# Optimization experiments

Measured on AMD Instinct MI355X. Metric: run time of the kernel, lower is better.

## Reference

```python
import jax, jax.numpy as jnp
import numpy as np

KEEP_H = 0.9   # zoneout_h keep prob (eval: deterministic mix)
KEEP_C = 0.5   # zoneout_c keep prob
F_BIAS = 1.0   # forget gate bias
EPS = 1e-5


def _ln(x, g, b):
    mu = x.mean(-1, keepdims=True)
    v = x.var(-1, keepdims=True)
    return (x - mu) * jax.lax.rsqrt(v + EPS) * g + b


def _ln4(z, g, b, h):
    # layer-norm each of the 4 gate chunks independently
    B = z.shape[0]
    z4 = z.reshape(B, 4, h)
    mu = z4.mean(-1, keepdims=True)
    v = z4.var(-1, keepdims=True)
    zn = ((z4 - mu) * jax.lax.rsqrt(v + EPS)).reshape(B, 4 * h)
    return zn * g + b


def _ln_lstm_cell(x, h, c, W, b, gg, bg, gc, bc):
    hu = h.shape[1]
    z = _ln4(jnp.concatenate([x, h], axis=1) @ W + b, gg, bg, hu)
    i, j, f, o = jnp.split(z, 4, axis=1)
    new_c = c * jax.nn.sigmoid(f + F_BIAS) + jax.nn.sigmoid(i) * jnp.tanh(j)
    new_h = jnp.tanh(_ln(new_c, gc, bc)) * jax.nn.sigmoid(o)
    # zoneout, eval mode (deterministic expectation)
    new_h = KEEP_H * new_h + (1.0 - KEEP_H) * h
    new_c = KEEP_C * new_c + (1.0 - KEEP_C) * c
    return new_h, new_c


def setup_inputs() -> dict:
    key = jax.random.key(0)
    ks = jax.random.split(key, 6)
    B, T, E, F, S, V = 128, 100, 128, 700, 400, 10000
    w = lambda k, shape: (jax.random.normal(k, shape, jnp.float32) * 0.06)
    return {
        "inputs": jax.random.normal(ks[0], (B, T, E), jnp.float32),
        "W0": w(ks[1], (E + F, 4 * F)), "b0": jnp.zeros((4 * F,), jnp.float32),
        "g0": jnp.ones((4 * F,), jnp.float32), "bg0": jnp.zeros((4 * F,), jnp.float32),
        "gc0": jnp.ones((F,), jnp.float32), "bc0": jnp.zeros((F,), jnp.float32),
        "W1": w(ks[2], (S + F, 4 * F)), "b1": jnp.zeros((4 * F,), jnp.float32),
        "g1": jnp.ones((4 * F,), jnp.float32), "bg1": jnp.zeros((4 * F,), jnp.float32),
        "gc1": jnp.ones((F,), jnp.float32), "bc1": jnp.zeros((F,), jnp.float32),
        "WS": w(ks[3], (F + S, 4 * S)), "bS": jnp.zeros((4 * S,), jnp.float32),
        "gS": jnp.ones((4 * S,), jnp.float32), "bgS": jnp.zeros((4 * S,), jnp.float32),
        "gcS": jnp.ones((S,), jnp.float32), "bcS": jnp.zeros((S,), jnp.float32),
        "Wout": w(ks[4], (F, V)), "bout": jnp.zeros((V,), jnp.float32),
    }


def reference(inputs, W0, b0, g0, bg0, gc0, bc0,
              W1, b1, g1, bg1, gc1, bc1,
              WS, bS, gS, bgS, gcS, bcS, Wout, bout):
    B, T, E = inputs.shape
    F = gc0.shape[0]
    S = gcS.shape[0]
    xs = inputs.transpose(1, 0, 2)  # [T, B, E]
    init = (jnp.zeros((B, F), inputs.dtype), jnp.zeros((B, F), inputs.dtype),
            jnp.zeros((B, S), inputs.dtype), jnp.zeros((B, S), inputs.dtype))

    def step(carry, xt):
        fh, fc, sh, sc = carry
        fh, fc = _ln_lstm_cell(xt, fh, fc, W0, b0, g0, bg0, gc0, bc0)  # Fast cell 0
        sh, sc = _ln_lstm_cell(fh, sh, sc, WS, bS, gS, bgS, gcS, bcS)  # Slow cell
        fh, fc = _ln_lstm_cell(sh, fh, fc, W1, b1, g1, bg1, gc1, bc1)  # Fast cell 1
        return (fh, fc, sh, sc), fh

    (fh, fc, sh, sc), outs = jax.lax.scan(step, init, xs)  # outs: [T, B, F]
    # torch: cat(outputs, dim=1).view(-1, F) == reshape of [B, T, F]
    flat = outs.transpose(1, 0, 2).reshape(B * T, F)
    logits = (flat @ Wout + bout).reshape(T, B, -1)  # torch .view([T, B, V])
    return (logits, fh, fc, sh, sc)
```

## Files before the change

### kernel.cpp

```cpp
#include <hip/hip_runtime.h>
#include <math.h>


#define B_ 128
#define T_ 100
#define E_ 128
#define F_ 700
#define S_ 400
#define V_ 10000

#define FP_ 704
#define SP_ 416
#define G_  256
#define TPB_ 512

#define W0_TILE_B 45056
#define KW_TILE_B 71680
#define LDS_BYTES 143360

using v8s = __attribute__((ext_vector_type(8))) short;
using v4f = __attribute__((ext_vector_type(4))) float;
typedef unsigned short u16;

#define NTL(p)    __builtin_nontemporal_load((p))

__device__ __forceinline__ void stcohf(float* p, float v) {
    asm volatile("global_store_dword %0, %1, off sc0 sc1" :: "v"(p), "v"(v) : "memory");
}
__device__ __forceinline__ void stcohs(u16* p, u16 v) {
    unsigned w = v;
    asm volatile("global_store_short %0, %1, off sc0 sc1" :: "v"(p), "v"(w) : "memory");
}

__device__ __forceinline__ u16 f2bf(float x) {
    unsigned int u = __float_as_uint(x);
    u += 0x7FFFu + ((u >> 16) & 1u);
    return (u16)(u >> 16);
}
__device__ __forceinline__ float bf2f(u16 h) {
    return __uint_as_float(((unsigned int)h) << 16);
}
__device__ __forceinline__ void split3f(float x, u16& h, u16& m, u16& l) {
    h = f2bf(x); float r  = x - bf2f(h);
    m = f2bf(r); float r2 = r - bf2f(m);
    l = f2bf(r2);
}
__device__ __forceinline__ float sigm(float x) { return 1.0f / (1.0f + expf(-x)); }

__device__ __forceinline__ void gbar(unsigned* flags, unsigned* go, unsigned target) {
    asm volatile("s_waitcnt vmcnt(0)" ::: "memory");
    __syncthreads();
    if (threadIdx.x == 0) {
        __hip_atomic_store(flags + (size_t)blockIdx.x * 16, target,
                           __ATOMIC_RELAXED, __HIP_MEMORY_SCOPE_AGENT);
        asm volatile("buffer_inv sc0 sc1" ::: "memory");
    }
    if (blockIdx.x == 0) {
        if (threadIdx.x < G_) {
            const unsigned* f = flags + (size_t)threadIdx.x * 16;
            while (__hip_atomic_load(f, __ATOMIC_RELAXED, __HIP_MEMORY_SCOPE_AGENT) < target)
                __builtin_amdgcn_s_sleep(1);
        }
        __syncthreads();
        if (threadIdx.x == 0)
            __hip_atomic_store(go, target, __ATOMIC_RELAXED, __HIP_MEMORY_SCOPE_AGENT);
    } else {
        if (threadIdx.x == 0) {
            while (__hip_atomic_load(go, __ATOMIC_RELAXED, __HIP_MEMORY_SCOPE_AGENT) < target)
                __builtin_amdgcn_s_sleep(1);
        }
    }
    __syncthreads();
}

__global__ __launch_bounds__(256) void wtrans3(
    const float* __restrict__ W, int K, int N,
    u16* __restrict__ WtH, u16* __restrict__ WtM, u16* __restrict__ WtL,
    int Kp, int K1, int K1pad)
{
    __shared__ float t[32][33];
    const int c0 = blockIdx.x * 32, kp0 = blockIdx.y * 32;
    const int tx = threadIdx.x & 31, ty = threadIdx.x >> 5;
    #pragma unroll
    for (int i = 0; i < 4; ++i) {
        int kpos = kp0 + ty + i * 8, c = c0 + tx;
        int k = (kpos < K1) ? kpos : (kpos >= K1pad ? K1 + (kpos - K1pad) : -1);
        t[ty + i * 8][tx] = (k >= 0 && k < K && c < N) ? W[(size_t)k * N + c] : 0.f;
    }
    __syncthreads();
    #pragma unroll
    for (int i = 0; i < 4; ++i) {
        int r = c0 + ty + i * 8;
        u16 h, m, l;
        split3f(t[tx][ty + i * 8], h, m, l);
        size_t idx = (size_t)r * Kp + kp0 + tx;
        WtH[idx] = h; WtM[idx] = m; WtL[idx] = l;
    }
}

__global__ __launch_bounds__(256) void wtrans(
    const float* __restrict__ W, int K, int N,
    u16* __restrict__ Wt, int Kpad)
{
    __shared__ float t[32][33];
    const int c0 = blockIdx.x * 32, k0 = blockIdx.y * 32;
    const int tx = threadIdx.x & 31, ty = threadIdx.x >> 5;
    #pragma unroll
    for (int i = 0; i < 4; ++i) {
        int k = k0 + ty + i * 8, c = c0 + tx;
        t[ty + i * 8][tx] = (k < K && c < N) ? W[(size_t)k * N + c] : 0.f;
    }
    __syncthreads();
    #pragma unroll
    for (int i = 0; i < 4; ++i) {
        int r = c0 + ty + i * 8;
        Wt[(size_t)r * Kpad + k0 + tx] = f2bf(t[tx][ty + i * 8]);
    }
}

__global__ __launch_bounds__(512, 1) void zxpre(
    const float* __restrict__ inputs,
    const u16* __restrict__ WH, const u16* __restrict__ WM,
    const u16* __restrict__ WL, const float* __restrict__ b0,
    float* __restrict__ zx)
{
    const int lane = threadIdx.x & 63, wid = threadIdx.x >> 6;
    const int lo = lane & 15, hi = lane >> 4;
    const int ntiles = 175 * 100;
    for (int i = blockIdx.x * 8 + wid; i < ntiles; i += gridDim.x * 8) {
        const int t = i / 175, ct = i % 175;
        v4f acc[8];
        #pragma unroll
        for (int m = 0; m < 8; ++m) acc[m] = (v4f)0.f;
        const size_t bb = (size_t)(ct * 16 + lo) * 832 + hi * 8;
        for (int kt = 0; kt < 4; ++kt) {
            const size_t bo = bb + kt * 32;
            v8s bh = *(const v8s*)(WH + bo);
            v8s bm = *(const v8s*)(WM + bo);
            v8s bl = *(const v8s*)(WL + bo);
            #pragma unroll
            for (int m = 0; m < 8; ++m) {
                const float* p = inputs + (size_t)(m * 16 + lo) * (T_ * E_)
                               + (size_t)t * E_ + kt * 32 + hi * 8;
                float v0[8];
                *(float4*)(v0)     = *(const float4*)(p);
                *(float4*)(v0 + 4) = *(const float4*)(p + 4);
                v8s ah, am, al;
                #pragma unroll
                for (int j = 0; j < 8; ++j) {
                    u16 H, M, L; split3f(v0[j], H, M, L);
                    ah[j] = (short)H; am[j] = (short)M; al[j] = (short)L;
                }
                acc[m] = __builtin_amdgcn_mfma_f32_16x16x32_bf16(ah, bh, acc[m], 0, 0, 0);
                acc[m] = __builtin_amdgcn_mfma_f32_16x16x32_bf16(ah, bm, acc[m], 0, 0, 0);
                acc[m] = __builtin_amdgcn_mfma_f32_16x16x32_bf16(am, bh, acc[m], 0, 0, 0);
                acc[m] = __builtin_amdgcn_mfma_f32_16x16x32_bf16(ah, bl, acc[m], 0, 0, 0);
                acc[m] = __builtin_amdgcn_mfma_f32_16x16x32_bf16(al, bh, acc[m], 0, 0, 0);
                acc[m] = __builtin_amdgcn_mfma_f32_16x16x32_bf16(am, bm, acc[m], 0, 0, 0);
            }
        }
        const int col = ct * 16 + lo;
        const float bb0 = b0[col];
        #pragma unroll
        for (int m = 0; m < 8; ++m)
            #pragma unroll
            for (int r = 0; r < 4; ++r) {
                int row = m * 16 + hi * 4 + r;
                zx[((size_t)t * B_ + row) * 2800 + col] = acc[m][r] + bb0;
            }
    }
}

__device__ void fill_tile(char* dst, const u16* __restrict__ H,
                          const u16* __restrict__ M, int Kp, int gcol0, int NT)
{
    const int n = 16 * NT * 4;
    for (int idx = threadIdx.x; idx < n; idx += TPB_) {
        const int c   = idx & 3;
        const int kt  = (idx >> 2) % NT;
        const int col = (idx >> 2) / NT;
        const size_t g = (size_t)(gcol0 + col) * Kp + kt * 32 + c * 8;
        const int o = kt * 2048 + col * 64 + c * 16;
        *(v8s*)(dst + o)        = *(const v8s*)(H + g);
        *(v8s*)(dst + o + 1024) = *(const v8s*)(M + g);
    }
}

__device__ void gemm_lds(
    const char* lt, int NT,
    const u16* __restrict__ A1H, const u16* __restrict__ A1M,
    const u16* __restrict__ A1L, int lda1, int K1pad,
    const u16* __restrict__ A2H, const u16* __restrict__ A2M,
    const u16* __restrict__ A2L, int lda2,
    const u16* __restrict__ WL, int KpL, int col0,
    const float* __restrict__ bias, const float* __restrict__ zadd,
    float* __restrict__ z, int N)
{
    const int lane = threadIdx.x & 63;
    const int lo = lane & 15, hi = lane >> 4;
    const int r0 = (threadIdx.x >> 6) * 16;
    v4f acc = (v4f)0.f;
    const u16* blp = WL + (size_t)(col0 + lo) * KpL + hi * 8;
    const size_t arow = (size_t)(r0 + lo);

    v8s aH[3], aM[3], aL[3], bL[3];
    #pragma unroll
    for (int s = 0; s < 3; ++s) {
        const int kb2 = s * 32;
        const bool s1 = kb2 < K1pad;
        const size_t ao = arow * (s1 ? lda1 : lda2)
                        + (s1 ? kb2 : kb2 - K1pad) + hi * 8;
        aH[s] = *(const v8s*)((s1 ? A1H : A2H) + ao);
        aM[s] = *(const v8s*)((s1 ? A1M : A2M) + ao);
        aL[s] = *(const v8s*)((s1 ? A1L : A2L) + ao);
        bL[s] = *(const v8s*)(blp + kb2);
    }

    for (int kt0 = 0; kt0 < NT; kt0 += 3) {
        #pragma unroll
        for (int j = 0; j < 3; ++j) {
            const int kt = kt0 + j;
            if (kt < NT) {
                const int lb = kt * 2048 + lo * 64 + hi * 16;
                v8s bh = *(const v8s*)(lt + lb);
                v8s bm = *(const v8s*)(lt + lb + 1024);
                acc = __builtin_amdgcn_mfma_f32_16x16x32_bf16(aH[j], bh,    acc, 0, 0, 0);
                acc = __builtin_amdgcn_mfma_f32_16x16x32_bf16(aH[j], bm,    acc, 0, 0, 0);
                acc = __builtin_amdgcn_mfma_f32_16x16x32_bf16(aM[j], bh,    acc, 0, 0, 0);
                acc = __builtin_amdgcn_mfma_f32_16x16x32_bf16(aH[j], bL[j], acc, 0, 0, 0);
                acc = __builtin_amdgcn_mfma_f32_16x16x32_bf16(aL[j], bh,    acc, 0, 0, 0);
                acc = __builtin_amdgcn_mfma_f32_16x16x32_bf16(aM[j], bm,    acc, 0, 0, 0);
                const int kn = kt + 3;
                if (kn < NT) {
                    const int kb2 = kn * 32;
                    const bool s1 = kb2 < K1pad;
                    const size_t ao = arow * (s1 ? lda1 : lda2)
                                    + (s1 ? kb2 : kb2 - K1pad) + hi * 8;
                    aH[j] = *(const v8s*)((s1 ? A1H : A2H) + ao);
                    aM[j] = *(const v8s*)((s1 ? A1M : A2M) + ao);
                    aL[j] = *(const v8s*)((s1 ? A1L : A2L) + ao);
                    bL[j] = *(const v8s*)(blp + kb2);
                }
            }
        }
    }

    const int col = col0 + lo;
    if (zadd) {
        #pragma unroll
        for (int r = 0; r < 4; ++r) {
            int row = r0 + hi * 4 + r;
            float za = NTL(&zadd[(size_t)row * N + col]);
            stcohf(&z[(size_t)row * N + col], acc[r] + za);
        }
    } else {
        const float bv = bias[col];
        #pragma unroll
        for (int r = 0; r < 4; ++r) {
            int row = r0 + hi * 4 + r;
            stcohf(&z[(size_t)row * N + col], acc[r] + bv);
        }
    }
}

template <int NV>
__device__ __forceinline__ void blockSumN(float* v, float* red) {
    const int w = threadIdx.x >> 6, lane = threadIdx.x & 63;
    #pragma unroll
    for (int k = 0; k < NV; ++k) {
        float x = v[k];
        #pragma unroll
        for (int off = 32; off > 0; off >>= 1) x += __shfl_down(x, off, 64);
        v[k] = x;
    }
    __syncthreads();
    if (lane == 0) {
        #pragma unroll
        for (int k = 0; k < NV; ++k) red[k * 8 + w] = v[k];
    }
    __syncthreads();
    #pragma unroll
    for (int k = 0; k < NV; ++k) {
        float r = 0.f;
        #pragma unroll
        for (int j = 0; j < 8; ++j) r += red[k * 8 + j];
        v[k] = r;
    }
    __syncthreads();
}

template <int FF>
__device__ void pw_phase(const float* __restrict__ z,
    const float* __restrict__ gg, const float* __restrict__ bg,
    const float* __restrict__ gc, const float* __restrict__ bc,
    float* __restrict__ h, float* __restrict__ c,
    u16* __restrict__ hpH, u16* __restrict__ hpM, u16* __restrict__ hpL,
    int hstride, u16* __restrict__ hist, int t, float* red)
{
    const int tid = threadIdx.x;
    constexpr int NU = (FF + TPB_ - 1) / TPB_;
    for (int b = blockIdx.x; b < B_; b += G_) {
        const float* zr = z + (size_t)b * 4 * FF;
        float* hr = h + (size_t)b * FF;
        float* cr = c + (size_t)b * FF;

        float sv[8] = {0, 0, 0, 0, 0, 0, 0, 0};
        #pragma unroll
        for (int i = 0; i < NU; ++i) {
            int u = tid + i * TPB_;
            if (u < FF) {
                #pragma unroll
                for (int g = 0; g < 4; ++g) {
                    float v = NTL(&zr[g * FF + u]);
                    sv[g] += v; sv[4 + g] += v * v;
                }
            }
        }
        blockSumN<8>(sv, red);
        float mu[4], rs[4];
        #pragma unroll
        for (int g = 0; g < 4; ++g) {
            mu[g] = sv[g] / FF;
            rs[g] = rsqrtf(sv[4 + g] / FF - mu[g] * mu[g] + 1e-5f);
        }

        float nc[NU], og[NU], ho[NU], co[NU];
        float cv[2] = {0, 0};
        #pragma unroll
        for (int i = 0; i < NU; ++i) {
            int u = tid + i * TPB_;
            if (u < FF) {
                float zi = (NTL(&zr[u])          - mu[0]) * rs[0] * gg[u]          + bg[u];
                float zj = (NTL(&zr[FF + u])     - mu[1]) * rs[1] * gg[FF + u]     + bg[FF + u];
                float zf = (NTL(&zr[2 * FF + u]) - mu[2]) * rs[2] * gg[2 * FF + u] + bg[2 * FF + u];
                float zo = (NTL(&zr[3 * FF + u]) - mu[3]) * rs[3] * gg[3 * FF + u] + bg[3 * FF + u];
                float cold = cr[u];
                float ncv = cold * sigm(zf + 1.0f) + sigm(zi) * tanhf(zj);
                nc[i] = ncv; og[i] = sigm(zo); co[i] = cold; ho[i] = hr[u];
                cv[0] += ncv; cv[1] += ncv * ncv;
            } else { nc[i] = 0.f; og[i] = 0.f; co[i] = 0.f; ho[i] = 0.f; }
        }
        blockSumN<2>(cv, red);
        float muc = cv[0] / FF;
        float rsc = rsqrtf(cv[1] / FF - muc * muc + 1e-5f);

        #pragma unroll
        for (int i = 0; i < NU; ++i) {
            int u = tid + i * TPB_;
            if (u < FF) {
                float nh = tanhf((nc[i] - muc) * rsc * gc[u] + bc[u]) * og[i];
                float hout = 0.9f * nh + 0.1f * ho[i];
                float cout = 0.5f * nc[i] + 0.5f * co[i];
                stcohf(&hr[u], hout);
                stcohf(&cr[u], cout);
                u16 H, M, L;
                split3f(hout, H, M, L);
                size_t po = (size_t)b * hstride + u;
                stcohs(&hpH[po], H); stcohs(&hpM[po], M); stcohs(&hpL[po], L);
                if (hist) stcohs(&hist[((size_t)b * T_ + t) * FP_ + u], H);
            }
        }
        if (hist && tid < FP_ - FF)
            stcohs(&hist[((size_t)b * T_ + t) * FP_ + FF + tid], (u16)0);
    }
}

__global__ __launch_bounds__(TPB_) void mega(
    const float* __restrict__ b0, const float* __restrict__ g0,
    const float* __restrict__ bg0, const float* __restrict__ gc0,
    const float* __restrict__ bc0,
    const float* __restrict__ b1, const float* __restrict__ g1,
    const float* __restrict__ bg1, const float* __restrict__ gc1,
    const float* __restrict__ bc1,
    const float* __restrict__ bS, const float* __restrict__ gS,
    const float* __restrict__ bgS, const float* __restrict__ gcS,
    const float* __restrict__ bcS,
    const float* __restrict__ zx,
    float* fh, float* fc, float* sh, float* sc, float* z, u16* hist,
    u16* fhH, u16* fhM, u16* fhL, u16* shH, u16* shM, u16* shL,
    u16* W0H, u16* W0M, u16* W0L, u16* WSH, u16* WSM, u16* WSL,
    u16* W1H, u16* W1M, u16* W1L,
    float* outTail, unsigned* flags, unsigned* go)
{
    extern __shared__ char lds[];
    __shared__ float red[64];
    const int b = blockIdx.x;
    const int gtid = blockIdx.x * TPB_ + threadIdx.x;
    unsigned tgt = 0;

    if (b <= 174) {
        fill_tile(lds, W0H + 128, W0M + 128, 832, b * 16, 22);
        if (b <= 155) fill_tile(lds + W0_TILE_B, W1H, W1M, 1120, b * 16, 35);
        else          fill_tile(lds + W0_TILE_B, WSH, WSM, 1120, (b - 156) * 16, 35);
    } else {
        fill_tile(lds, WSH, WSM, 1120, (b - 156) * 16, 35);
        if (b <= 193)
            fill_tile(lds + KW_TILE_B, W1H, W1M, 1120, (156 + b - 175) * 16, 35);
    }
    __syncthreads();

    for (int t = 0; t < T_; ++t) {
        if (b <= 174)
            gemm_lds(lds, 22,
                     fhH, fhM, fhL, FP_, FP_, fhH, fhM, fhL, FP_,
                     W0L + 128, 832, b * 16,
                     nullptr, zx + (size_t)t * B_ * 2800, z, 2800);
        gbar(flags, go, ++tgt);
        pw_phase<F_>(z, g0, bg0, gc0, bc0, fh, fc, fhH, fhM, fhL, FP_, nullptr, 0, red);
        gbar(flags, go, ++tgt);
        if (b >= 156)
            gemm_lds(lds + (b <= 174 ? W0_TILE_B : 0), 35,
                     fhH, fhM, fhL, FP_, FP_, shH, shM, shL, SP_,
                     WSL, 1120, (b - 156) * 16,
                     bS, nullptr, z, 1600);
        gbar(flags, go, ++tgt);
        pw_phase<S_>(z, gS, bgS, gcS, bcS, sh, sc, shH, shM, shL, SP_, nullptr, 0, red);
        gbar(flags, go, ++tgt);
        if (b <= 155)
            gemm_lds(lds + W0_TILE_B, 35,
                     shH, shM, shL, SP_, SP_, fhH, fhM, fhL, FP_,
                     W1L, 1120, b * 16, b1, nullptr, z, 2800);
        else if (b >= 175 && b <= 193)
            gemm_lds(lds + KW_TILE_B, 35,
                     shH, shM, shL, SP_, SP_, fhH, fhM, fhL, FP_,
                     W1L, 1120, (156 + b - 175) * 16, b1, nullptr, z, 2800);
        gbar(flags, go, ++tgt);
        pw_phase<F_>(z, g1, bg1, gc1, bc1, fh, fc, fhH, fhM, fhL, FP_, hist, t, red);
        gbar(flags, go, ++tgt);
    }

    const int NF = B_ * F_, NS = B_ * S_;
    for (int i = gtid; i < 2 * NF + 2 * NS; i += G_ * TPB_) {
        float v = (i < NF) ? fh[i] : (i < 2 * NF) ? fc[i - NF]
                : (i < 2 * NF + NS) ? sh[i - 2 * NF] : sc[i - 2 * NF - NS];
        stcohf(&outTail[i], v);
    }
}

__global__ __launch_bounds__(512) void ogemm(
    const u16* __restrict__ A, const u16* __restrict__ Bt,
    const float* __restrict__ bias, float* __restrict__ C)
{
    const int N = V_;
    const int tid = threadIdx.x, lane = tid & 63, wid = tid >> 6;
    const int wm = wid >> 1, wn = wid & 1;
    const int row0 = blockIdx.y * 256 + wm * 64;
    const int col0 = blockIdx.x * 128 + wn * 64;
    const int lo = lane & 15, hi = lane >> 4;
    const int NT = FP_ / 32;

    v4f acc[4][4];
    #pragma unroll
    for (int i = 0; i < 4; ++i)
        #pragma unroll
        for (int j = 0; j < 4; ++j) acc[i][j] = (v4f)0.f;

    for (int kt = 0; kt < NT; ++kt) {
        const int kb = kt * 32 + hi * 8;
        v8s a[4], bfr[4];
        #pragma unroll
        for (int i = 0; i < 4; ++i) {
            a[i]   = *(const v8s*)(A  + (size_t)(row0 + i * 16 + lo) * FP_ + kb);
            bfr[i] = *(const v8s*)(Bt + (size_t)(col0 + i * 16 + lo) * FP_ + kb);
        }
        #pragma unroll
        for (int mf = 0; mf < 4; ++mf)
            #pragma unroll
            for (int nf = 0; nf < 4; ++nf)
                acc[mf][nf] = __builtin_amdgcn_mfma_f32_16x16x32_bf16(a[mf], bfr[nf], acc[mf][nf], 0, 0, 0);
    }

    #pragma unroll
    for (int mf = 0; mf < 4; ++mf) {
        #pragma unroll
        for (int nf = 0; nf < 4; ++nf) {
            int col = col0 + nf * 16 + lo;
            if (col < N) {
                float bb = bias[col];
                #pragma unroll
                for (int r = 0; r < 4; ++r) {
                    int row = row0 + mf * 16 + hi * 4 + r;
                    C[(size_t)row * N + col] = acc[mf][nf][r] + bb;
                }
            }
        }
    }
}

extern "C" void kernel_launch(void* const* d_in, const int* in_sizes, int n_in,
                              void* d_out, int out_size, void* d_ws, size_t ws_size,
                              hipStream_t stream) {
    const float* inputs = (const float*)d_in[0];
    const float* W0   = (const float*)d_in[1];
    const float* b0   = (const float*)d_in[2];
    const float* g0   = (const float*)d_in[3];
    const float* bg0  = (const float*)d_in[4];
    const float* gc0  = (const float*)d_in[5];
    const float* bc0  = (const float*)d_in[6];
    const float* W1   = (const float*)d_in[7];
    const float* b1   = (const float*)d_in[8];
    const float* g1   = (const float*)d_in[9];
    const float* bg1  = (const float*)d_in[10];
    const float* gc1  = (const float*)d_in[11];
    const float* bc1  = (const float*)d_in[12];
    const float* WS   = (const float*)d_in[13];
    const float* bS   = (const float*)d_in[14];
    const float* gS   = (const float*)d_in[15];
    const float* bgS  = (const float*)d_in[16];
    const float* gcS  = (const float*)d_in[17];
    const float* bcS  = (const float*)d_in[18];
    const float* Wout = (const float*)d_in[19];
    const float* bout = (const float*)d_in[20];

    float* ws = (float*)d_ws;
    float* fh = ws;
    float* fc = fh + B_ * F_;
    float* sh = fc + B_ * F_;
    float* sc = sh + B_ * S_;
    float* z  = sc + B_ * S_;
    u16* hist = (u16*)(z + (size_t)B_ * 4 * F_);
    u16* Wtout = hist + (size_t)12800 * FP_;
    unsigned* flags = (unsigned*)(Wtout + (size_t)10112 * FP_);
    unsigned* go    = flags + G_ * 16;

    const size_t P0 = (size_t)2816 * 832;
    const size_t PS = (size_t)1664 * 1120;
    const size_t P1 = (size_t)2816 * 1120;
    const size_t HF = (size_t)B_ * FP_;
    const size_t HS = (size_t)B_ * SP_;
    u16* dp  = (u16*)d_out;
    u16* W0H = dp;          u16* W0M = W0H + P0;  u16* W0L = W0M + P0;
    u16* WSH = W0L + P0;    u16* WSM = WSH + PS;  u16* WSL = WSM + PS;
    u16* W1H = WSL + PS;    u16* W1M = W1H + P1;  u16* W1L = W1M + P1;
    u16* fhH = W1L + P1;    u16* fhM = fhH + HF;  u16* fhL = fhM + HF;
    u16* shH = fhL + HF;    u16* shM = shH + HS;  u16* shL = shM + HS;
    float* zx = (float*)(shL + HS);

    hipMemsetAsync(flags, 0, (G_ * 16 + 16) * sizeof(unsigned), stream);
    hipMemsetAsync(fh, 0, (size_t)(2 * B_ * F_ + 2 * B_ * S_) * sizeof(float), stream);
    hipMemsetAsync(fhH, 0, (3 * HF + 3 * HS) * sizeof(u16), stream);

    wtrans3<<<dim3(88, 26), 256, 0, stream>>>(W0, E_ + F_, 4 * F_, W0H, W0M, W0L, 832, 128, 128);
    wtrans3<<<dim3(52, 35), 256, 0, stream>>>(WS, F_ + S_, 4 * S_, WSH, WSM, WSL, 1120, F_, FP_);
    wtrans3<<<dim3(88, 35), 256, 0, stream>>>(W1, S_ + F_, 4 * F_, W1H, W1M, W1L, 1120, S_, SP_);
    wtrans<<<dim3(316, 22), 256, 0, stream>>>(Wout, F_, V_, Wtout, FP_);

    zxpre<<<2188, 512, 0, stream>>>(inputs, W0H, W0M, W0L, b0, zx);

    hipFuncSetAttribute((const void*)mega,
                        hipFuncAttributeMaxDynamicSharedMemorySize, LDS_BYTES);

    mega<<<G_, TPB_, LDS_BYTES, stream>>>(
        b0, g0, bg0, gc0, bc0,
        b1, g1, bg1, gc1, bc1,
        bS, gS, bgS, gcS, bcS,
        zx,
        fh, fc, sh, sc, z, hist,
        fhH, fhM, fhL, shH, shM, shL,
        W0H, W0M, W0L, WSH, WSM, WSL, W1H, W1M, W1L,
        (float*)d_out + (size_t)B_ * T_ * V_, flags, go);

    ogemm<<<dim3(79, 50), 512, 0, stream>>>(hist, Wtout, bout, (float*)d_out);
}
```

Measured before the change: 11.44 ms.

## Replace centralized grid barrier with all-to-all flag polling and swizzle LDS tiles

The grid barrier no longer routes through block 0 and a shared go flag. Every block now polls all 256 per-block flags directly, which removes one serialized hop (block 0 observing then publishing) from each of the six barriers per timestep. Separately, the LDS weight-tile layout gets an XOR swizzle on the 16-byte chunk index to cut bank conflicts on the MFMA B-operand reads. The trade-off is heavier polling traffic on the flag lines, since every block now reads all flags.

```diff
diff --git a/kernel.cpp b/kernel.cpp
--- a/kernel.cpp
+++ b/kernel.cpp
@@ -47,28 +47,18 @@
 }
 __device__ __forceinline__ float sigm(float x) { return 1.0f / (1.0f + expf(-x)); }
 
-__device__ __forceinline__ void gbar(unsigned* flags, unsigned* go, unsigned target) {
+__device__ __forceinline__ void gbar(unsigned* flags, unsigned target) {
     asm volatile("s_waitcnt vmcnt(0)" ::: "memory");
     __syncthreads();
-    if (threadIdx.x == 0) {
+    if (threadIdx.x == 0)
         __hip_atomic_store(flags + (size_t)blockIdx.x * 16, target,
                            __ATOMIC_RELAXED, __HIP_MEMORY_SCOPE_AGENT);
-        asm volatile("buffer_inv sc0 sc1" ::: "memory");
-    }
-    if (blockIdx.x == 0) {
-        if (threadIdx.x < G_) {
-            const unsigned* f = flags + (size_t)threadIdx.x * 16;
-            while (__hip_atomic_load(f, __ATOMIC_RELAXED, __HIP_MEMORY_SCOPE_AGENT) < target)
-                __builtin_amdgcn_s_sleep(1);
-        }
-        __syncthreads();
-        if (threadIdx.x == 0)
-            __hip_atomic_store(go, target, __ATOMIC_RELAXED, __HIP_MEMORY_SCOPE_AGENT);
-    } else {
-        if (threadIdx.x == 0) {
-            while (__hip_atomic_load(go, __ATOMIC_RELAXED, __HIP_MEMORY_SCOPE_AGENT) < target)
-                __builtin_amdgcn_s_sleep(1);
-        }
+    if (threadIdx.x == 256)
+        asm volatile("buffer_inv sc0 sc1\n\ts_waitcnt vmcnt(0)" ::: "memory");
+    if (threadIdx.x < G_) {
+        const unsigned* f = flags + (size_t)threadIdx.x * 16;
+        while (__hip_atomic_load(f, __ATOMIC_RELAXED, __HIP_MEMORY_SCOPE_AGENT) < target)
+            __builtin_amdgcn_s_sleep(1);
     }
     __syncthreads();
 }
@@ -180,7 +170,7 @@
         const int kt  = (idx >> 2) % NT;
         const int col = (idx >> 2) / NT;
         const size_t g = (size_t)(gcol0 + col) * Kp + kt * 32 + c * 8;
-        const int o = kt * 2048 + col * 64 + c * 16;
+        const int o = kt * 2048 + col * 64 + ((c ^ ((col >> 1) & 3)) * 16);
         *(v8s*)(dst + o)        = *(const v8s*)(H + g);
         *(v8s*)(dst + o + 1024) = *(const v8s*)(M + g);
     }
@@ -202,6 +192,7 @@
     v4f acc = (v4f)0.f;
     const u16* blp = WL + (size_t)(col0 + lo) * KpL + hi * 8;
     const size_t arow = (size_t)(r0 + lo);
+    const int csw = (hi ^ ((lo >> 1) & 3)) << 4;
 
     v8s aH[3], aM[3], aL[3], bL[3];
     #pragma unroll
@@ -221,7 +212,7 @@
         for (int j = 0; j < 3; ++j) {
             const int kt = kt0 + j;
             if (kt < NT) {
-                const int lb = kt * 2048 + lo * 64 + hi * 16;
+                const int lb = kt * 2048 + lo * 64 + csw;
                 v8s bh = *(const v8s*)(lt + lb);
                 v8s bm = *(const v8s*)(lt + lb + 1024);
                 acc = __builtin_amdgcn_mfma_f32_16x16x32_bf16(aH[j], bh,    acc, 0, 0, 0);
@@ -380,7 +371,7 @@
     u16* fhH, u16* fhM, u16* fhL, u16* shH, u16* shM, u16* shL,
     u16* W0H, u16* W0M, u16* W0L, u16* WSH, u16* WSM, u16* WSL,
     u16* W1H, u16* W1M, u16* W1L,
-    float* outTail, unsigned* flags, unsigned* go)
+    float* outTail, unsigned* flags)
 {
     extern __shared__ char lds[];
     __shared__ float red[64];
@@ -405,17 +396,17 @@
                      fhH, fhM, fhL, FP_, FP_, fhH, fhM, fhL, FP_,
                      W0L + 128, 832, b * 16,
                      nullptr, zx + (size_t)t * B_ * 2800, z, 2800);
-        gbar(flags, go, ++tgt);
+        gbar(flags, ++tgt);
         pw_phase<F_>(z, g0, bg0, gc0, bc0, fh, fc, fhH, fhM, fhL, FP_, nullptr, 0, red);
-        gbar(flags, go, ++tgt);
+        gbar(flags, ++tgt);
         if (b >= 156)
             gemm_lds(lds + (b <= 174 ? W0_TILE_B : 0), 35,
                      fhH, fhM, fhL, FP_, FP_, shH, shM, shL, SP_,
                      WSL, 1120, (b - 156) * 16,
                      bS, nullptr, z, 1600);
-        gbar(flags, go, ++tgt);
+        gbar(flags, ++tgt);
         pw_phase<S_>(z, gS, bgS, gcS, bcS, sh, sc, shH, shM, shL, SP_, nullptr, 0, red);
-        gbar(flags, go, ++tgt);
+        gbar(flags, ++tgt);
         if (b <= 155)
             gemm_lds(lds + W0_TILE_B, 35,
                      shH, shM, shL, SP_, SP_, fhH, fhM, fhL, FP_,
@@ -424,9 +415,9 @@
             gemm_lds(lds + KW_TILE_B, 35,
                      shH, shM, shL, SP_, SP_, fhH, fhM, fhL, FP_,
                      W1L, 1120, (156 + b - 175) * 16, b1, nullptr, z, 2800);
-        gbar(flags, go, ++tgt);
+        gbar(flags, ++tgt);
         pw_phase<F_>(z, g1, bg1, gc1, bc1, fh, fc, fhH, fhM, fhL, FP_, hist, t, red);
-        gbar(flags, go, ++tgt);
+        gbar(flags, ++tgt);
     }
 
     const int NF = B_ * F_, NS = B_ * S_;
@@ -521,7 +512,6 @@
     u16* hist = (u16*)(z + (size_t)B_ * 4 * F_);
     u16* Wtout = hist + (size_t)12800 * FP_;
     unsigned* flags = (unsigned*)(Wtout + (size_t)10112 * FP_);
-    unsigned* go    = flags + G_ * 16;
 
     const size_t P0 = (size_t)2816 * 832;
     const size_t PS = (size_t)1664 * 1120;
@@ -558,7 +548,7 @@
         fh, fc, sh, sc, z, hist,
         fhH, fhM, fhL, shH, shM, shL,
         W0H, W0M, W0L, WSH, WSM, WSL, W1H, W1M, W1L,
-        (float*)d_out + (size_t)B_ * T_ * V_, flags, go);
+        (float*)d_out + (size_t)B_ * T_ * V_, flags);
 
     ogemm<<<dim3(79, 50), 512, 0, stream>>>(hist, Wtout, bout, (float*)d_out);
 }
```

After: 11.44 ms. Within noise of the previous version (+0.0%).
